# Optimization experiments

Measured on AMD Instinct MI355X. Metric: run time of the kernel, lower is better.

The kernel has to match this reference:

```python
import jax, jax.numpy as jnp
import numpy as np
import math

N = 64
DIN = 2
DOUT = 2
D = 4
BATCH = 16384
EPS_DIV = 1e-6


def setup_inputs() -> dict:
    key = jax.random.key(0)
    k1, k2, k3 = jax.random.split(key, 3)
    x = jax.random.normal(k1, (BATCH, N, DIN), jnp.float32)
    # A scaled by 0.5 to keep 64-step products of DxD matrices inside float32 range
    A = jax.random.normal(k2, (N, D, D, DIN), jnp.float32) * 0.5
    B = jax.random.normal(k3, (N, D, D, DOUT, DIN), jnp.float32)
    scale = jnp.ones((1,), jnp.float32)
    return {"x": x, "A": A, "B": B, "scale": scale}


def _forward(x, A, B, scale):
    b, n, din = x.shape
    nbin = int(math.log(n - 1) / math.log(2.0)) + 1  # matches torch set_parallel_vars
    s = scale.reshape(())
    # per-site L2 normalization of input features (torch: X / ||X||, no eps)
    xn = x / jnp.linalg.norm(x, axis=-1, keepdims=True)
    M = jnp.einsum('bni,nlri->nblr', xn, A)  # [n, b, D, D] site matrices
    # binary tree of pairwise products: levels[l] has (n >> l) blocks covering 2^l sites
    levels = [M]
    cur = M
    for _ in range(nbin - 1):
        m = cur.shape[0]
        pair = cur.reshape(m // 2, 2, b, D, D)
        cur = jnp.einsum('pbij,pbjk->pbik', pair[:, 0], pair[:, 1])
        levels.append(cur)
    idx = jnp.arange(n)
    # Left prefix boundary vectors: vL[i] = e0^T * prod_{k<i} M_k (i=0 unused).
    # Built by walking the set bits of i (MSB->LSB), exactly like the torch
    # Bleft[nbin-1-j][xp[j]] indexing, but vectorized over all i at once.
    vL = jnp.zeros((n, b, D), M.dtype)
    startedL = jnp.zeros((n,), bool)
    for j in range(nbin):
        l = nbin - 1 - j                 # tree level for bit j
        bit = ((idx >> l) & 1).astype(bool)
        blk = 2 * (idx >> (l + 1))       # == xp[j] in torch
        Bl = levels[l][blk]              # [n, b, D, D]
        init = Bl[:, :, 0, :]            # left boundary row e0^T A
        step = jnp.einsum('nbi,nbij->nbj', vL, Bl)
        new = jnp.where(startedL[:, None, None], step, init)
        vL = jnp.where(bit[:, None, None], new, vL)
        startedL = startedL | bit
    vL = vL / (jnp.linalg.norm(vL, axis=-1, keepdims=True) + EPS_DIV)
    # Right suffix boundary vectors: vR[i] = (prod_{k=n-i}^{n-1} M_k) e0 (i=0 unused).
    # For n a power of two, Bright levels coincide with Bleft levels.
    vR = jnp.zeros((n, b, D), M.dtype)
    startedR = jnp.zeros((n,), bool)
    for j in range(nbin):
        l = nbin - 1 - j
        bit = ((idx >> l) & 1).astype(bool)
        nblk = n >> l
        blk = nblk - 1 - 2 * (idx >> (l + 1))  # index from the right end
        Bl = levels[l][blk]
        init = Bl[:, :, :, 0]            # right boundary column A e0
        step = jnp.einsum('nbij,nbj->nbi', Bl, vR)
        new = jnp.where(startedR[:, None, None], step, init)
        vR = jnp.where(bit[:, None, None], new, vR)
        startedR = startedR | bit
    vR = vR / (jnp.linalg.norm(vR, axis=-1, keepdims=True) + EPS_DIV)
    Aright = vR[::-1]  # Aright[i] = vR[n-1-i], valid for sites 0..n-2
    # Local operators H_i: boundary-contracted MPO tensors
    Hmid = jnp.einsum('nbi,niljk,nbl->nbjk', vL[1:n - 1], B[1:n - 1], Aright[1:n - 1])
    H0 = jnp.einsum('ljk,bl->bjk', B[0, 0], Aright[0])
    Hlast = jnp.einsum('bi,ijk->bjk', vL[n - 1], B[n - 1, :, 0])
    H = jnp.concatenate([H0[None], Hmid, Hlast[None]], axis=0)  # [n, b, dout, din]
    nrm = jnp.sqrt(jnp.sum(H * H, axis=(-2, -1), keepdims=True)) + EPS_DIV
    H = s * (H / nrm)
    H = jnp.where(jnp.isnan(H), 0.0, H)
    H = jax.nn.relu(H)                   # activation='relu'
    # apply local operator to normalized local input; out_norm='none'
    y = jnp.einsum('nbjk,bnk->bnj', H, xn)  # [b, n, dout]
    return y


def reference(x, A, B, scale):
    return _forward(x, A, B, scale)
```

## Files before the change

kernel.cpp:

```cpp
#include <hip/hip_runtime.h>
#include <math.h>


#define RSQ(x) __builtin_amdgcn_rsqf((x) + 1e-30f)

__global__ __launch_bounds__(1024, 4)
void tdvp_kernel(const float* __restrict__ x,
                 const float* __restrict__ A,
                 const float* __restrict__ Bw,
                 const float* __restrict__ scale,
                 float* __restrict__ y)
{
    __shared__ float sU[16384];

    const int tid = threadIdx.x;
    const int bb  = tid & 63;
    const int s   = __builtin_amdgcn_readfirstlane(tid >> 6);

    {
        const float4* xg = (const float4*)x + (size_t)blockIdx.x * 2048;
        #pragma unroll
        for (int it = 0; it < 2; ++it) {
            const int g = it * 1024 + tid;
            const float4 v = xg[g];
            const int c = g >> 5, f = (g & 31) * 4;
            *(float2*)&sU[c * 130 + f]     = make_float2(v.x, v.y);
            *(float2*)&sU[c * 130 + f + 2] = make_float2(v.z, v.w);
        }
    }
    __syncthreads();

    const int n0 = s * 4;
    float xa[4], xc[4];
    #pragma unroll
    for (int k = 0; k < 4; ++k) {
        const float2 v = *(const float2*)&sU[bb * 130 + n0 * 2 + 2 * k];
        const float inr = RSQ(v.x * v.x + v.y * v.y);
        xa[k] = v.x * inr; xc[k] = v.y * inr;
    }
    __syncthreads();

    float M[4][16];
    #pragma unroll
    for (int k = 0; k < 4; ++k) {
        const float* Ak = A + (size_t)(n0 + k) * 32;
        #pragma unroll
        for (int e = 0; e < 16; ++e)
            M[k][e] = fmaf(xc[k], Ak[2*e+1], xa[k] * Ak[2*e]);
    }

    {
        float P[16];
        #pragma unroll
        for (int e = 0; e < 16; ++e) P[e] = M[0][e];
        #pragma unroll
        for (int k = 1; k < 4; ++k) {
            float Pn[16];
            #pragma unroll
            for (int i = 0; i < 4; ++i) {
                #pragma unroll
                for (int j = 0; j < 4; ++j) {
                    float acc = P[i*4] * M[k][j];
                    acc = fmaf(P[i*4+1], M[k][4+j],  acc);
                    acc = fmaf(P[i*4+2], M[k][8+j],  acc);
                    acc = fmaf(P[i*4+3], M[k][12+j], acc);
                    Pn[i*4+j] = acc;
                }
            }
            #pragma unroll
            for (int e = 0; e < 16; ++e) P[e] = Pn[e];
        }
        float ss = 0.f;
        #pragma unroll
        for (int e = 0; e < 16; ++e) ss = fmaf(P[e], P[e], ss);
        const float rn = RSQ(ss);
        #pragma unroll
        for (int q = 0; q < 4; ++q)
            *(float4*)&sU[s * 1024 + q * 256 + bb * 4] =
                make_float4(P[4*q]*rn, P[4*q+1]*rn, P[4*q+2]*rn, P[4*q+3]*rn);
    }
    __syncthreads();

    float v0 = 1.f, v1 = 0.f, v2 = 0.f, v3 = 0.f;
    float u0 = 1.f, u1 = 0.f, u2 = 0.f, u3 = 0.f;
    const int nsuf = 15 - s;
    #pragma unroll 1
    for (int i = 0; i < 15; ++i) {
        if (i < s) {
            const float4* pp = (const float4*)&sU[i * 1024 + bb * 4];
            const float4 r0 = pp[0], r1 = pp[64], r2 = pp[128], r3 = pp[192];
            const float w0 = v0*r0.x + v1*r1.x + v2*r2.x + v3*r3.x;
            const float w1 = v0*r0.y + v1*r1.y + v2*r2.y + v3*r3.y;
            const float w2 = v0*r0.z + v1*r1.z + v2*r2.z + v3*r3.z;
            const float w3 = v0*r0.w + v1*r1.w + v2*r2.w + v3*r3.w;
            v0 = w0; v1 = w1; v2 = w2; v3 = w3;
        }
        if (i < nsuf) {
            const float4* pp = (const float4*)&sU[(15 - i) * 1024 + bb * 4];
            const float4 r0 = pp[0], r1 = pp[64], r2 = pp[128], r3 = pp[192];
            const float w0 = r0.x*u0 + r0.y*u1 + r0.z*u2 + r0.w*u3;
            const float w1 = r1.x*u0 + r1.y*u1 + r1.z*u2 + r1.w*u3;
            const float w2 = r2.x*u0 + r2.y*u1 + r2.z*u2 + r2.w*u3;
            const float w3 = r3.x*u0 + r3.y*u1 + r3.z*u2 + r3.w*u3;
            u0 = w0; u1 = w1; u2 = w2; u3 = w3;
        }
    }

    float vlA[4], vlB[4], vlC[4], vlD[4];
    {
        float a0 = v0, a1 = v1, a2 = v2, a3 = v3;
        #pragma unroll
        for (int k = 0; k < 4; ++k) {
            vlA[k] = a0; vlB[k] = a1; vlC[k] = a2; vlD[k] = a3;
            if (k == 3) break;
            const float t0 = a0*M[k][0] + a1*M[k][4] + a2*M[k][8]  + a3*M[k][12];
            const float t1 = a0*M[k][1] + a1*M[k][5] + a2*M[k][9]  + a3*M[k][13];
            const float t2 = a0*M[k][2] + a1*M[k][6] + a2*M[k][10] + a3*M[k][14];
            const float t3 = a0*M[k][3] + a1*M[k][7] + a2*M[k][11] + a3*M[k][15];
            a0 = t0; a1 = t1; a2 = t2; a3 = t3;
        }
    }
    __syncthreads();

    const float sc = scale[0];
    #pragma unroll
    for (int kk = 3; kk >= 0; --kk) {
        const int n = n0 + kk;

        const float arn = RSQ(u0*u0 + u1*u1 + u2*u2 + u3*u3);
        float aa0 = u0*arn, aa1 = u1*arn, aa2 = u2*arn, aa3 = u3*arn;
        if (n == 63) { aa0 = 1.f; aa1 = aa2 = aa3 = 0.f; }

        const float wn = RSQ(vlA[kk]*vlA[kk] + vlB[kk]*vlB[kk] +
                             vlC[kk]*vlC[kk] + vlD[kk]*vlD[kk]);
        float vv0 = vlA[kk]*wn, vv1 = vlB[kk]*wn, vv2 = vlC[kk]*wn, vv3 = vlD[kk]*wn;
        if (n == 0) { vv0 = 1.f; vv1 = vv2 = vv3 = 0.f; }

        const float vv[4] = {vv0, vv1, vv2, vv3};
        const float aa[4] = {aa0, aa1, aa2, aa3};
        const float* Bn = Bw + (size_t)n * 64;
        float H00 = 0.f, H01 = 0.f, H10 = 0.f, H11 = 0.f;
        #pragma unroll
        for (int i = 0; i < 4; ++i) {
            #pragma unroll
            for (int l = 0; l < 4; ++l) {
                const float c = vv[i] * aa[l];
                const int   q = (i * 4 + l) * 4;
                H00 = fmaf(c, Bn[q + 0], H00);
                H01 = fmaf(c, Bn[q + 1], H01);
                H10 = fmaf(c, Bn[q + 2], H10);
                H11 = fmaf(c, Bn[q + 3], H11);
            }
        }
        const float rh = sc * RSQ(H00*H00 + H01*H01 + H10*H10 + H11*H11);
        H00 *= rh; H01 *= rh; H10 *= rh; H11 *= rh;
        if (__builtin_isnan(H00)) H00 = 0.f;
        if (__builtin_isnan(H01)) H01 = 0.f;
        if (__builtin_isnan(H10)) H10 = 0.f;
        if (__builtin_isnan(H11)) H11 = 0.f;
        H00 = fmaxf(H00, 0.f); H01 = fmaxf(H01, 0.f);
        H10 = fmaxf(H10, 0.f); H11 = fmaxf(H11, 0.f);

        float2 yo;
        yo.x = fmaf(H01, xc[kk], H00 * xa[kk]);
        yo.y = fmaf(H11, xc[kk], H10 * xa[kk]);
        *(float2*)&sU[bb * 130 + 2 * n] = yo;

        if (kk > 0) {
            const float t0 = M[kk][0]*u0  + M[kk][1]*u1  + M[kk][2]*u2  + M[kk][3]*u3;
            const float t1 = M[kk][4]*u0  + M[kk][5]*u1  + M[kk][6]*u2  + M[kk][7]*u3;
            const float t2 = M[kk][8]*u0  + M[kk][9]*u1  + M[kk][10]*u2 + M[kk][11]*u3;
            const float t3 = M[kk][12]*u0 + M[kk][13]*u1 + M[kk][14]*u2 + M[kk][15]*u3;
            u0 = t0; u1 = t1; u2 = t2; u3 = t3;
        }
    }
    __syncthreads();

    {
        float4* yg = (float4*)y + (size_t)blockIdx.x * 2048;
        #pragma unroll
        for (int it = 0; it < 2; ++it) {
            const int g = it * 1024 + tid;
            const int c = g >> 5, f = (g & 31) * 4;
            const float2 a = *(const float2*)&sU[c * 130 + f];
            const float2 b = *(const float2*)&sU[c * 130 + f + 2];
            yg[g] = make_float4(a.x, a.y, b.x, b.y);
        }
    }
}

extern "C" void kernel_launch(void* const* d_in, const int* in_sizes, int n_in,
                              void* d_out, int out_size, void* d_ws, size_t ws_size,
                              hipStream_t stream) {
    const float* x     = (const float*)d_in[0];
    const float* A     = (const float*)d_in[1];
    const float* B     = (const float*)d_in[2];
    const float* scale = (const float*)d_in[3];
    float* yp = (float*)d_out;
    const int batch  = in_sizes[0] / 128;
    const int blocks = batch / 64;
    tdvp_kernel<<<blocks, 1024, 0, stream>>>(x, A, B, scale, yp);
}
```

Before: 75.75 us.

## Halve block size, stage A/B weights in LDS, load x directly to registers

Blocks now cover 32 batch rows with 512 threads instead of 64 rows with 1024 threads. The A and B weight tables are staged once into shared memory and read back as float4. Each thread now loads its own x slice and writes its own y slice straight to global memory, which removes the LDS transpose and two barriers. The prefix/suffix loop is also fully unrolled. The trade-offs are strided, less coalesced global accesses (each thread touches 32 bytes at a 512-byte stride) and more register pressure from the unrolled loop.

```diff
diff --git a/kernel.cpp b/kernel.cpp
--- a/kernel.cpp
+++ b/kernel.cpp
@@ -4,49 +4,50 @@
 
 #define RSQ(x) __builtin_amdgcn_rsqf((x) + 1e-30f)
 
-__global__ __launch_bounds__(1024, 4)
+__global__ __launch_bounds__(512, 4)
 void tdvp_kernel(const float* __restrict__ x,
                  const float* __restrict__ A,
                  const float* __restrict__ Bw,
                  const float* __restrict__ scale,
                  float* __restrict__ y)
 {
-    __shared__ float sU[16384];
+    __shared__ float sA[2048];
+    __shared__ float sB[4096];
+    __shared__ float sP[8192];
 
     const int tid = threadIdx.x;
-    const int bb  = tid & 63;
-    const int s   = __builtin_amdgcn_readfirstlane(tid >> 6);
+    const int bb  = tid & 31;
+    const int s   = tid >> 5;
 
-    {
-        const float4* xg = (const float4*)x + (size_t)blockIdx.x * 2048;
-        #pragma unroll
-        for (int it = 0; it < 2; ++it) {
-            const int g = it * 1024 + tid;
-            const float4 v = xg[g];
-            const int c = g >> 5, f = (g & 31) * 4;
-            *(float2*)&sU[c * 130 + f]     = make_float2(v.x, v.y);
-            *(float2*)&sU[c * 130 + f + 2] = make_float2(v.z, v.w);
-        }
-    }
-    __syncthreads();
+    ((float4*)sA)[tid]       = ((const float4*)A)[tid];
+    ((float4*)sB)[tid]       = ((const float4*)Bw)[tid];
+    ((float4*)sB)[512 + tid] = ((const float4*)Bw)[512 + tid];
 
     const int n0 = s * 4;
+    const float* xp = x + (size_t)blockIdx.x * 4096 + bb * 128 + n0 * 2;
+    const float4 xv0 = *(const float4*)xp;
+    const float4 xv1 = *(const float4*)(xp + 4);
     float xa[4], xc[4];
-    #pragma unroll
-    for (int k = 0; k < 4; ++k) {
-        const float2 v = *(const float2*)&sU[bb * 130 + n0 * 2 + 2 * k];
-        const float inr = RSQ(v.x * v.x + v.y * v.y);
-        xa[k] = v.x * inr; xc[k] = v.y * inr;
+    {
+        float r;
+        r = RSQ(xv0.x*xv0.x + xv0.y*xv0.y); xa[0]=xv0.x*r; xc[0]=xv0.y*r;
+        r = RSQ(xv0.z*xv0.z + xv0.w*xv0.w); xa[1]=xv0.z*r; xc[1]=xv0.w*r;
+        r = RSQ(xv1.x*xv1.x + xv1.y*xv1.y); xa[2]=xv1.x*r; xc[2]=xv1.y*r;
+        r = RSQ(xv1.z*xv1.z + xv1.w*xv1.w); xa[3]=xv1.z*r; xc[3]=xv1.w*r;
     }
+
     __syncthreads();
 
     float M[4][16];
     #pragma unroll
     for (int k = 0; k < 4; ++k) {
-        const float* Ak = A + (size_t)(n0 + k) * 32;
+        const float4* Aq = (const float4*)&sA[(n0 + k) * 32];
         #pragma unroll
-        for (int e = 0; e < 16; ++e)
-            M[k][e] = fmaf(xc[k], Ak[2*e+1], xa[k] * Ak[2*e]);
+        for (int t = 0; t < 8; ++t) {
+            const float4 q = Aq[t];
+            M[k][2*t]   = fmaf(xc[k], q.y, xa[k] * q.x);
+            M[k][2*t+1] = fmaf(xc[k], q.w, xa[k] * q.z);
+        }
     }
 
     {
@@ -76,7 +77,7 @@
         const float rn = RSQ(ss);
         #pragma unroll
         for (int q = 0; q < 4; ++q)
-            *(float4*)&sU[s * 1024 + q * 256 + bb * 4] =
+            *(float4*)&sP[s * 512 + q * 128 + bb * 4] =
                 make_float4(P[4*q]*rn, P[4*q+1]*rn, P[4*q+2]*rn, P[4*q+3]*rn);
     }
     __syncthreads();
@@ -84,11 +85,11 @@
     float v0 = 1.f, v1 = 0.f, v2 = 0.f, v3 = 0.f;
     float u0 = 1.f, u1 = 0.f, u2 = 0.f, u3 = 0.f;
     const int nsuf = 15 - s;
-    #pragma unroll 1
+    #pragma unroll
     for (int i = 0; i < 15; ++i) {
         if (i < s) {
-            const float4* pp = (const float4*)&sU[i * 1024 + bb * 4];
-            const float4 r0 = pp[0], r1 = pp[64], r2 = pp[128], r3 = pp[192];
+            const float4* pp = (const float4*)&sP[i * 512 + bb * 4];
+            const float4 r0 = pp[0], r1 = pp[32], r2 = pp[64], r3 = pp[96];
             const float w0 = v0*r0.x + v1*r1.x + v2*r2.x + v3*r3.x;
             const float w1 = v0*r0.y + v1*r1.y + v2*r2.y + v3*r3.y;
             const float w2 = v0*r0.z + v1*r1.z + v2*r2.z + v3*r3.z;
@@ -96,8 +97,8 @@
             v0 = w0; v1 = w1; v2 = w2; v3 = w3;
         }
         if (i < nsuf) {
-            const float4* pp = (const float4*)&sU[(15 - i) * 1024 + bb * 4];
-            const float4 r0 = pp[0], r1 = pp[64], r2 = pp[128], r3 = pp[192];
+            const float4* pp = (const float4*)&sP[(15 - i) * 512 + bb * 4];
+            const float4 r0 = pp[0], r1 = pp[32], r2 = pp[64], r3 = pp[96];
             const float w0 = r0.x*u0 + r0.y*u1 + r0.z*u2 + r0.w*u3;
             const float w1 = r1.x*u0 + r1.y*u1 + r1.z*u2 + r1.w*u3;
             const float w2 = r2.x*u0 + r2.y*u1 + r2.z*u2 + r2.w*u3;
@@ -120,9 +121,9 @@
             a0 = t0; a1 = t1; a2 = t2; a3 = t3;
         }
     }
-    __syncthreads();
 
     const float sc = scale[0];
+    float yr[8];
     #pragma unroll
     for (int kk = 3; kk >= 0; --kk) {
         const int n = n0 + kk;
@@ -138,19 +139,22 @@
 
         const float vv[4] = {vv0, vv1, vv2, vv3};
         const float aa[4] = {aa0, aa1, aa2, aa3};
-        const float* Bn = Bw + (size_t)n * 64;
+        const float4* Bq = (const float4*)&sB[n * 64];
         float H00 = 0.f, H01 = 0.f, H10 = 0.f, H11 = 0.f;
         #pragma unroll
         for (int i = 0; i < 4; ++i) {
-            #pragma unroll
-            for (int l = 0; l < 4; ++l) {
-                const float c = vv[i] * aa[l];
-                const int   q = (i * 4 + l) * 4;
-                H00 = fmaf(c, Bn[q + 0], H00);
-                H01 = fmaf(c, Bn[q + 1], H01);
-                H10 = fmaf(c, Bn[q + 2], H10);
-                H11 = fmaf(c, Bn[q + 3], H11);
-            }
+            const float4 b0 = Bq[i*4+0], b1 = Bq[i*4+1],
+                         b2 = Bq[i*4+2], b3 = Bq[i*4+3];
+            const float c0 = vv[i]*aa[0], c1 = vv[i]*aa[1],
+                        c2 = vv[i]*aa[2], c3 = vv[i]*aa[3];
+            H00 = fmaf(c0, b0.x, H00); H01 = fmaf(c0, b0.y, H01);
+            H10 = fmaf(c0, b0.z, H10); H11 = fmaf(c0, b0.w, H11);
+            H00 = fmaf(c1, b1.x, H00); H01 = fmaf(c1, b1.y, H01);
+            H10 = fmaf(c1, b1.z, H10); H11 = fmaf(c1, b1.w, H11);
+            H00 = fmaf(c2, b2.x, H00); H01 = fmaf(c2, b2.y, H01);
+            H10 = fmaf(c2, b2.z, H10); H11 = fmaf(c2, b2.w, H11);
+            H00 = fmaf(c3, b3.x, H00); H01 = fmaf(c3, b3.y, H01);
+            H10 = fmaf(c3, b3.z, H10); H11 = fmaf(c3, b3.w, H11);
         }
         const float rh = sc * RSQ(H00*H00 + H01*H01 + H10*H10 + H11*H11);
         H00 *= rh; H01 *= rh; H10 *= rh; H11 *= rh;
@@ -161,10 +165,8 @@
         H00 = fmaxf(H00, 0.f); H01 = fmaxf(H01, 0.f);
         H10 = fmaxf(H10, 0.f); H11 = fmaxf(H11, 0.f);
 
-        float2 yo;
-        yo.x = fmaf(H01, xc[kk], H00 * xa[kk]);
-        yo.y = fmaf(H11, xc[kk], H10 * xa[kk]);
-        *(float2*)&sU[bb * 130 + 2 * n] = yo;
+        yr[2*kk]     = fmaf(H01, xc[kk], H00 * xa[kk]);
+        yr[2*kk + 1] = fmaf(H11, xc[kk], H10 * xa[kk]);
 
         if (kk > 0) {
             const float t0 = M[kk][0]*u0  + M[kk][1]*u1  + M[kk][2]*u2  + M[kk][3]*u3;
@@ -174,18 +176,11 @@
             u0 = t0; u1 = t1; u2 = t2; u3 = t3;
         }
     }
-    __syncthreads();
 
     {
-        float4* yg = (float4*)y + (size_t)blockIdx.x * 2048;
-        #pragma unroll
-        for (int it = 0; it < 2; ++it) {
-            const int g = it * 1024 + tid;
-            const int c = g >> 5, f = (g & 31) * 4;
-            const float2 a = *(const float2*)&sU[c * 130 + f];
-            const float2 b = *(const float2*)&sU[c * 130 + f + 2];
-            yg[g] = make_float4(a.x, a.y, b.x, b.y);
-        }
+        float* yp = y + (size_t)blockIdx.x * 4096 + bb * 128 + n0 * 2;
+        *(float4*)yp       = make_float4(yr[0], yr[1], yr[2], yr[3]);
+        *(float4*)(yp + 4) = make_float4(yr[4], yr[5], yr[6], yr[7]);
     }
 }
 
@@ -198,6 +193,6 @@
     const float* scale = (const float*)d_in[3];
     float* yp = (float*)d_out;
     const int batch  = in_sizes[0] / 128;
-    const int blocks = batch / 64;
-    tdvp_kernel<<<blocks, 1024, 0, stream>>>(x, A, B, scale, yp);
+    const int blocks = batch / 32;
+    tdvp_kernel<<<blocks, 512, 0, stream>>>(x, A, B, scale, yp);
 }
```

New measurement: 79.44 us. +4.9%, slower.
